# Performance work log

Hardware: AMD Instinct MI355X
Metric: run time of the kernel (lower is better)

## Reference

```python
import jax, jax.numpy as jnp
import numpy as np

B, S1, S2 = 1024, 25, 10          # batch, hop-1 fanout, hop-2 fanout
N, D, H, C = 100000, 256, 128, 64  # n_node, in_dim, per-branch out_dim, n_class


def setup_inputs() -> dict:
    key = jax.random.key(0)
    ks = jax.random.split(key, 10)
    rn = lambda k, shape: jax.random.normal(k, shape, dtype=jnp.float32) * 0.05
    return {
        "ids0": jax.random.randint(ks[0], (B,), 0, N),
        "ids1": jax.random.randint(ks[1], (B * S1,), 0, N),
        "ids2": jax.random.randint(ks[2], (B * S1 * S2,), 0, N),
        "features": jax.random.normal(ks[3], (N, D), dtype=jnp.float32),
        # aggregator layer 1 (in D, out 2H after concat)
        "Wx1": rn(ks[4], (D, H)), "bx1": jnp.zeros((H,), jnp.float32),
        "Wn1": rn(ks[5], (D, H)), "bn1": jnp.zeros((H,), jnp.float32),
        # aggregator layer 2 (in 2H, out 2H)
        "Wx2": rn(ks[6], (2 * H, H)), "bx2": jnp.zeros((H,), jnp.float32),
        "Wn2": rn(ks[7], (2 * H, H)), "bn2": jnp.zeros((H,), jnp.float32),
        # final linear head
        "Wfc": rn(ks[8], (2 * H, C)), "bfc": jnp.zeros((C,), jnp.float32),
    }


def _mean_agg(x, neibs, Wx, bx, Wn, bn, act):
    # neibs: [x_rows * fanout, d] -> mean over fanout, then concat of two linears
    n = neibs.reshape(x.shape[0], -1, neibs.shape[-1]).mean(axis=1)
    out = jnp.concatenate([x @ Wx + bx, n @ Wn + bn], axis=-1)
    return act(out)


def reference(ids0, ids1, ids2, features,
              Wx1, bx1, Wn1, bn1, Wx2, bx2, Wn2, bn2, Wfc, bfc):
    # hop-wise feature gathers (identity prep)
    h0 = features[ids0]   # [B, D]
    h1 = features[ids1]   # [B*S1, D]
    h2 = features[ids2]   # [B*S1*S2, D]
    # layer 1 aggregation (relu), applied to consecutive hop pairs
    g0 = _mean_agg(h0, h1, Wx1, bx1, Wn1, bn1, jax.nn.relu)   # [B, 2H]
    g1 = _mean_agg(h1, h2, Wx1, bx1, Wn1, bn1, jax.nn.relu)   # [B*S1, 2H]
    # layer 2 aggregation (identity activation on last layer)
    f0 = _mean_agg(g0, g1, Wx2, bx2, Wn2, bn2, lambda v: v)   # [B, 2H]
    return f0 @ Wfc + bfc  # [B, C]
```

## Files before the change

### kernel.cpp

```cpp
#include <hip/hip_runtime.h>

#define DD 256
#define HH 128
#define CC 64
#define BB 1024
#define SS1 25
#define SS2 10
#define NN 100000

typedef __attribute__((ext_vector_type(8))) short bf16x8;
typedef __attribute__((ext_vector_type(4))) float f32x4;

__device__ inline unsigned short f2b(float x) {
    union { float f; unsigned u; } v; v.f = x;
    unsigned r = (v.u + 0x7fffu + ((v.u >> 16) & 1u)) >> 16;
    return (unsigned short)r;
}
__device__ inline float b2f(unsigned u16) {
    union { unsigned u; float f; } v; v.u = u16 << 16;
    return v.f;
}

__global__ __launch_bounds__(256)
void prep_w(const float* __restrict__ Wx, const float* __restrict__ Wn,
            unsigned short* __restrict__ Wsw) {
    const int t    = blockIdx.x * 256 + threadIdx.x;
    const int lane = t & 63;
    const int frag = t >> 6;
    const int kc = frag >> 4, nt = frag & 15;
    const int quad = lane >> 4, lr = lane & 15;
    unsigned short v[8];
#pragma unroll
    for (int j = 0; j < 8; ++j) {
        int k = kc * 32 + quad * 8 + j;
        int n = nt * 16 + lr;
        float w = (n < HH) ? Wx[k * HH + n] : Wn[k * HH + (n - HH)];
        v[j] = f2b(w);
    }
    ((uint4*)Wsw)[t] = *(uint4*)v;
}

#define PQ_BLOCKS 512
#define PQ_TILES  (NN / 32)
#define AS 264

__global__ __launch_bounds__(256, 2)
void pq_gemm(const float* __restrict__ feat,
             const unsigned short* __restrict__ Wsw,
             unsigned short* __restrict__ PQb) {
    __shared__ unsigned short sAO[2][32 * AS];
    const int t    = threadIdx.x;
    const int w    = t >> 6, lane = t & 63;
    const int quad = lane >> 4, lr = lane & 15;

    bf16x8 B[8][4];
#pragma unroll
    for (int kc = 0; kc < 8; ++kc)
#pragma unroll
        for (int j = 0; j < 4; ++j)
            B[kc][j] = *(const bf16x8*)&Wsw[((kc * 16 + (w * 4 + j)) * 64 + lane) * 8];

    const int srow = t >> 5, sc = t & 31;

    float4 v[8];
    {
        const float* fb = feat + (long)blockIdx.x * 32 * DD + sc * 8;
#pragma unroll
        for (int i = 0; i < 4; ++i) {
            const float4* src = (const float4*)(fb + (long)(i * 8 + srow) * DD);
            v[2 * i]     = src[0];
            v[2 * i + 1] = src[1];
        }
    }

#pragma unroll 1
    for (int tile = blockIdx.x; tile < PQ_TILES; tile += PQ_BLOCKS) {
#pragma unroll
        for (int i = 0; i < 4; ++i) {
            int row = i * 8 + srow;
            float4 a = v[2 * i], b = v[2 * i + 1];
            unsigned short w8[8] = { f2b(a.x), f2b(a.y), f2b(a.z), f2b(a.w),
                                     f2b(b.x), f2b(b.y), f2b(b.z), f2b(b.w) };
            *(uint4*)&sAO[0][row * AS + sc * 8] = *(uint4*)w8;
        }
        int tn = tile + PQ_BLOCKS;
        if (tn < PQ_TILES) {
            const float* fn = feat + (long)tn * 32 * DD + sc * 8;
#pragma unroll
            for (int i = 0; i < 4; ++i) {
                const float4* src = (const float4*)(fn + (long)(i * 8 + srow) * DD);
                v[2 * i]     = src[0];
                v[2 * i + 1] = src[1];
            }
        }
        asm volatile("s_waitcnt lgkmcnt(0)" ::: "memory");
        __builtin_amdgcn_s_barrier();

        f32x4 acc[2][4] = {};
#pragma unroll
        for (int kc = 0; kc < 8; ++kc) {
            bf16x8 a0 = *(const bf16x8*)&sAO[0][(lr)      * AS + kc * 32 + quad * 8];
            bf16x8 a1 = *(const bf16x8*)&sAO[0][(16 + lr) * AS + kc * 32 + quad * 8];
#pragma unroll
            for (int j = 0; j < 4; ++j) {
                acc[0][j] = __builtin_amdgcn_mfma_f32_16x16x32_bf16(a0, B[kc][j], acc[0][j], 0, 0, 0);
                acc[1][j] = __builtin_amdgcn_mfma_f32_16x16x32_bf16(a1, B[kc][j], acc[1][j], 0, 0, 0);
            }
        }
#pragma unroll
        for (int rt = 0; rt < 2; ++rt)
#pragma unroll
            for (int j = 0; j < 4; ++j) {
                int col = (w * 4 + j) * 16 + lr;
#pragma unroll
                for (int r = 0; r < 4; ++r)
                    sAO[1][(rt * 16 + quad * 4 + r) * AS + col] = f2b(acc[rt][j][r]);
            }
        asm volatile("s_waitcnt lgkmcnt(0)" ::: "memory");
        __builtin_amdgcn_s_barrier();

#pragma unroll
        for (int i = 0; i < 4; ++i) {
            int id  = i * 256 + t;
            int row = id >> 5, ch = id & 31;
            uint4 d = *(uint4*)&sAO[1][row * AS + ch * 8];
            *(uint4*)&PQb[((long)tile * 32 + row) * DD + ch * 8] = d;
        }
    }
}

__global__ __launch_bounds__(256)
void megatail(const unsigned short* __restrict__ PQb,
              const int* __restrict__ ids0, const int* __restrict__ ids1,
              const int* __restrict__ ids2,
              const float* __restrict__ bx1, const float* __restrict__ bn1,
              const float* __restrict__ Wx2, const float* __restrict__ bx2,
              const float* __restrict__ Wn2, const float* __restrict__ bn2,
              const float* __restrict__ Wfc, const float* __restrict__ bfc,
              float* __restrict__ out) {
    __shared__ float sred[8][3 * HH];
    __shared__ float g0L[DD];
    __shared__ float gmL[DD];
    __shared__ float FL[DD];
    __shared__ float sp[4][CC];
    const int i    = blockIdx.x;
    const int t    = threadIdx.x;
    const int wv   = t >> 6, lane = t & 63;
    const int sub  = lane >> 5, lr = lane & 31;
    const int slot = wv * 2 + sub;

    const float4 bx = *(const float4*)&bx1[lr * 4];
    const float4 bn = *(const float4*)&bn1[lr * 4];
    float4 xs  = {0.f, 0.f, 0.f, 0.f};
    float4 ns  = {0.f, 0.f, 0.f, 0.f};
    float4 g0n = {0.f, 0.f, 0.f, 0.f};

#pragma unroll
    for (int it = 0; it < 4; ++it) {
        int s = slot + it * 8;
        if (s < SS1) {
            int row  = i * SS1 + s;
            long xr  = (long)ids1[row];
            uint2 xv  = *(const uint2*)&PQb[xr * DD + lr * 4];
            uint2 nv0 = *(const uint2*)&PQb[xr * DD + HH + lr * 4];
            int myid = ids2[row * SS2 + (lr % SS2)];
            float4 acc = {0.f, 0.f, 0.f, 0.f};
#pragma unroll
            for (int j = 0; j < SS2; ++j) {
                long nr = (long)__shfl(myid, (lane & 32) + j);
                uint2 nv = *(const uint2*)&PQb[nr * DD + HH + lr * 4];
                acc.x += b2f(nv.x & 0xffff); acc.y += b2f(nv.x >> 16);
                acc.z += b2f(nv.y & 0xffff); acc.w += b2f(nv.y >> 16);
            }
            constexpr float inv2 = 1.f / SS2;
            xs.x += fmaxf(b2f(xv.x & 0xffff) + bx.x, 0.f);
            xs.y += fmaxf(b2f(xv.x >> 16)    + bx.y, 0.f);
            xs.z += fmaxf(b2f(xv.y & 0xffff) + bx.z, 0.f);
            xs.w += fmaxf(b2f(xv.y >> 16)    + bx.w, 0.f);
            ns.x += fmaxf(acc.x * inv2 + bn.x, 0.f);
            ns.y += fmaxf(acc.y * inv2 + bn.y, 0.f);
            ns.z += fmaxf(acc.z * inv2 + bn.z, 0.f);
            ns.w += fmaxf(acc.w * inv2 + bn.w, 0.f);
            g0n.x += b2f(nv0.x & 0xffff); g0n.y += b2f(nv0.x >> 16);
            g0n.z += b2f(nv0.y & 0xffff); g0n.w += b2f(nv0.y >> 16);
        }
    }
    *(float4*)&sred[slot][lr * 4]            = xs;
    *(float4*)&sred[slot][HH + lr * 4]       = ns;
    *(float4*)&sred[slot][2 * HH + lr * 4]   = g0n;
    __syncthreads();

    {
        float rsum = 0.f;
#pragma unroll
        for (int k = 0; k < 8; ++k) rsum += sred[k][t];
        gmL[t] = rsum * (1.f / SS1);
        float g0v;
        if (t < HH) {
            unsigned short u = PQb[(long)ids0[i] * DD + t];
            g0v = fmaxf(b2f(u) + bx1[t], 0.f);
        } else {
            float s2 = 0.f;
#pragma unroll
            for (int k = 0; k < 8; ++k) s2 += sred[k][2 * HH + (t - HH)];
            g0v = fmaxf(s2 * (1.f / SS1) + bn1[t - HH], 0.f);
        }
        g0L[t] = g0v;
    }
    __syncthreads();

    {
        const bool xhalf = (t < HH);
        const float* __restrict__ W    = xhalf ? Wx2 : Wn2;
        const float* __restrict__ srcL = xhalf ? g0L : gmL;
        const int cc = t & (HH - 1);
        float fa = 0.f;
#pragma unroll 8
        for (int k = 0; k < DD; ++k) fa += srcL[k] * W[k * HH + cc];
        fa += xhalf ? bx2[cc] : bn2[cc];
        FL[t] = fa;
    }
    __syncthreads();

    {
        const int col = t & (CC - 1), q = t >> 6;
        float p = 0.f;
#pragma unroll 8
        for (int k = q * 64; k < q * 64 + 64; ++k) p += FL[k] * Wfc[k * CC + col];
        sp[q][col] = p;
    }
    __syncthreads();
    if (t < CC)
        out[(long)i * CC + t] = sp[0][t] + sp[1][t] + sp[2][t] + sp[3][t] + bfc[t];
}

extern "C" void kernel_launch(void* const* d_in, const int* in_sizes, int n_in,
                              void* d_out, int out_size, void* d_ws, size_t ws_size,
                              hipStream_t stream) {
    const int*   ids0 = (const int*)d_in[0];
    const int*   ids1 = (const int*)d_in[1];
    const int*   ids2 = (const int*)d_in[2];
    const float* feat = (const float*)d_in[3];
    const float* Wx1  = (const float*)d_in[4];
    const float* bx1  = (const float*)d_in[5];
    const float* Wn1  = (const float*)d_in[6];
    const float* bn1  = (const float*)d_in[7];
    const float* Wx2  = (const float*)d_in[8];
    const float* bx2  = (const float*)d_in[9];
    const float* Wn2  = (const float*)d_in[10];
    const float* bn2  = (const float*)d_in[11];
    const float* Wfc  = (const float*)d_in[12];
    const float* bfc  = (const float*)d_in[13];
    float* out = (float*)d_out;

    unsigned short* PQb = (unsigned short*)d_ws;
    unsigned short* Wsw = PQb + (long)NN * DD;

    prep_w<<<32, 256, 0, stream>>>(Wx1, Wn1, Wsw);
    pq_gemm<<<PQ_BLOCKS, 256, 0, stream>>>(feat, Wsw, PQb);
    megatail<<<BB, 256, 0, stream>>>(PQb, ids0, ids1, ids2, bx1, bn1,
                                     Wx2, bx2, Wn2, bn2, Wfc, bfc, out);
}
```

Measured before the change: 218.8 us.

## Double-buffer feature prefetch in pq_gemm and widen megatail to 512 threads

The PQ GEMM loop now keeps two register buffers of feature rows and prefetches two tiles ahead, so global loads of the next-next tile overlap the current tile's conversion and MFMA work. The tail kernel moves to 512 threads per block, spreading the 25 neighbor slots across 16 half-wave slots and splitting the layer-2 and FC dot products into more partial sums. The cost is higher register pressure in pq_gemm (16 float4 prefetch registers instead of 8), which may reduce occupancy under launch_bounds(256,2). The tail kernel also gains an extra shared-memory reduction step and barrier.

```diff
diff --git a/kernel.cpp b/kernel.cpp
--- a/kernel.cpp
+++ b/kernel.cpp
@@ -44,6 +44,71 @@
 #define PQ_TILES  (NN / 32)
 #define AS 264
 
+#define PQ_ISSUE(VREG, TIDX)                                                  \
+    {                                                                         \
+        const float* fn_ = feat + (long)(TIDX) * 32 * DD + sc * 8;            \
+        _Pragma("unroll")                                                     \
+        for (int i_ = 0; i_ < 4; ++i_) {                                      \
+            const float4* s_ = (const float4*)(fn_ + (long)(i_ * 8 + srow) * DD); \
+            VREG[2 * i_]     = s_[0];                                         \
+            VREG[2 * i_ + 1] = s_[1];                                         \
+        }                                                                     \
+    }
+
+#define PQ_STEP(VREG)                                                         \
+    {                                                                         \
+              \
+        _Pragma("unroll")                                                     \
+        for (int i_ = 0; i_ < 4; ++i_) {                                      \
+            int row_ = i_ * 8 + srow;                                         \
+            float4 a_ = VREG[2 * i_], b_ = VREG[2 * i_ + 1];                  \
+            unsigned short w8_[8] = { f2b(a_.x), f2b(a_.y), f2b(a_.z), f2b(a_.w), \
+                                      f2b(b_.x), f2b(b_.y), f2b(b_.z), f2b(b_.w) }; \
+            *(uint4*)&sAO[0][row_ * AS + sc * 8] = *(uint4*)w8_;              \
+        }                                                                     \
+                                \
+        {                                                                     \
+            long t2_ = tile + 2L * PQ_BLOCKS;                                 \
+            if (t2_ < PQ_TILES) PQ_ISSUE(VREG, t2_);                          \
+        }                                                                     \
+                       \
+        asm volatile("s_waitcnt lgkmcnt(0)" ::: "memory");                    \
+        __builtin_amdgcn_s_barrier();                                         \
+                                          \
+        f32x4 acc[2][4] = {};                                                 \
+        _Pragma("unroll")                                                     \
+        for (int kc = 0; kc < 8; ++kc) {                                      \
+            bf16x8 a0 = *(const bf16x8*)&sAO[0][(lr)      * AS + kc * 32 + quad * 8]; \
+            bf16x8 a1 = *(const bf16x8*)&sAO[0][(16 + lr) * AS + kc * 32 + quad * 8]; \
+            _Pragma("unroll")                                                 \
+            for (int j = 0; j < 4; ++j) {                                     \
+                acc[0][j] = __builtin_amdgcn_mfma_f32_16x16x32_bf16(a0, B[kc][j], acc[0][j], 0, 0, 0); \
+                acc[1][j] = __builtin_amdgcn_mfma_f32_16x16x32_bf16(a1, B[kc][j], acc[1][j], 0, 0, 0); \
+            }                                                                 \
+        }                                                                     \
+                  \
+        _Pragma("unroll")                                                     \
+        for (int rt = 0; rt < 2; ++rt)                                        \
+            _Pragma("unroll")                                                 \
+            for (int j = 0; j < 4; ++j) {                                     \
+                int col_ = (w * 4 + j) * 16 + lr;                             \
+                _Pragma("unroll")                                             \
+                for (int r = 0; r < 4; ++r)                                   \
+                    sAO[1][(rt * 16 + quad * 4 + r) * AS + col_] = f2b(acc[rt][j][r]); \
+            }                                                                 \
+                  \
+        asm volatile("s_waitcnt lgkmcnt(0)" ::: "memory");                    \
+        __builtin_amdgcn_s_barrier();                                         \
+                                           \
+        _Pragma("unroll")                                                     \
+        for (int i_ = 0; i_ < 4; ++i_) {                                      \
+            int id_  = i_ * 256 + t;                                          \
+            int row_ = id_ >> 5, ch_ = id_ & 31;                              \
+            uint4 d_ = *(uint4*)&sAO[1][row_ * AS + ch_ * 8];                 \
+            *(uint4*)&PQb[((long)tile * 32 + row_) * DD + ch_ * 8] = d_;      \
+        }                                                                     \
+    }
+
 __global__ __launch_bounds__(256, 2)
 void pq_gemm(const float* __restrict__ feat,
              const unsigned short* __restrict__ Wsw,
@@ -62,74 +127,20 @@
 
     const int srow = t >> 5, sc = t & 31;
 
-    float4 v[8];
-    {
-        const float* fb = feat + (long)blockIdx.x * 32 * DD + sc * 8;
-#pragma unroll
-        for (int i = 0; i < 4; ++i) {
-            const float4* src = (const float4*)(fb + (long)(i * 8 + srow) * DD);
-            v[2 * i]     = src[0];
-            v[2 * i + 1] = src[1];
-        }
-    }
-
-#pragma unroll 1
-    for (int tile = blockIdx.x; tile < PQ_TILES; tile += PQ_BLOCKS) {
-#pragma unroll
-        for (int i = 0; i < 4; ++i) {
-            int row = i * 8 + srow;
-            float4 a = v[2 * i], b = v[2 * i + 1];
-            unsigned short w8[8] = { f2b(a.x), f2b(a.y), f2b(a.z), f2b(a.w),
-                                     f2b(b.x), f2b(b.y), f2b(b.z), f2b(b.w) };
-            *(uint4*)&sAO[0][row * AS + sc * 8] = *(uint4*)w8;
-        }
-        int tn = tile + PQ_BLOCKS;
-        if (tn < PQ_TILES) {
-            const float* fn = feat + (long)tn * 32 * DD + sc * 8;
-#pragma unroll
-            for (int i = 0; i < 4; ++i) {
-                const float4* src = (const float4*)(fn + (long)(i * 8 + srow) * DD);
-                v[2 * i]     = src[0];
-                v[2 * i + 1] = src[1];
-            }
-        }
-        asm volatile("s_waitcnt lgkmcnt(0)" ::: "memory");
-        __builtin_amdgcn_s_barrier();
-
-        f32x4 acc[2][4] = {};
-#pragma unroll
-        for (int kc = 0; kc < 8; ++kc) {
-            bf16x8 a0 = *(const bf16x8*)&sAO[0][(lr)      * AS + kc * 32 + quad * 8];
-            bf16x8 a1 = *(const bf16x8*)&sAO[0][(16 + lr) * AS + kc * 32 + quad * 8];
-#pragma unroll
-            for (int j = 0; j < 4; ++j) {
-                acc[0][j] = __builtin_amdgcn_mfma_f32_16x16x32_bf16(a0, B[kc][j], acc[0][j], 0, 0, 0);
-                acc[1][j] = __builtin_amdgcn_mfma_f32_16x16x32_bf16(a1, B[kc][j], acc[1][j], 0, 0, 0);
-            }
-        }
-#pragma unroll
-        for (int rt = 0; rt < 2; ++rt)
-#pragma unroll
-            for (int j = 0; j < 4; ++j) {
-                int col = (w * 4 + j) * 16 + lr;
-#pragma unroll
-                for (int r = 0; r < 4; ++r)
-                    sAO[1][(rt * 16 + quad * 4 + r) * AS + col] = f2b(acc[rt][j][r]);
-            }
-        asm volatile("s_waitcnt lgkmcnt(0)" ::: "memory");
-        __builtin_amdgcn_s_barrier();
-
-#pragma unroll
-        for (int i = 0; i < 4; ++i) {
-            int id  = i * 256 + t;
-            int row = id >> 5, ch = id & 31;
-            uint4 d = *(uint4*)&sAO[1][row * AS + ch * 8];
-            *(uint4*)&PQb[((long)tile * 32 + row) * DD + ch * 8] = d;
-        }
-    }
-}
-
-__global__ __launch_bounds__(256)
+    float4 va[8], vb[8];
+    long tile = blockIdx.x;
+    PQ_ISSUE(va, tile);
+    if (tile + PQ_BLOCKS < PQ_TILES) PQ_ISSUE(vb, tile + PQ_BLOCKS);
+
+    while (true) {
+        PQ_STEP(va);
+        tile += PQ_BLOCKS; if (tile >= PQ_TILES) break;
+        PQ_STEP(vb);
+        tile += PQ_BLOCKS; if (tile >= PQ_TILES) break;
+    }
+}
+
+__global__ __launch_bounds__(512)
 void megatail(const unsigned short* __restrict__ PQb,
               const int* __restrict__ ids0, const int* __restrict__ ids1,
               const int* __restrict__ ids2,
@@ -138,11 +149,12 @@
               const float* __restrict__ Wn2, const float* __restrict__ bn2,
               const float* __restrict__ Wfc, const float* __restrict__ bfc,
               float* __restrict__ out) {
-    __shared__ float sred[8][3 * HH];
+    __shared__ float sred[16][3 * HH];
     __shared__ float g0L[DD];
     __shared__ float gmL[DD];
+    __shared__ float FP[2][DD];
     __shared__ float FL[DD];
-    __shared__ float sp[4][CC];
+    __shared__ float sp[8][CC];
     const int i    = blockIdx.x;
     const int t    = threadIdx.x;
     const int wv   = t >> 6, lane = t & 63;
@@ -156,8 +168,8 @@
     float4 g0n = {0.f, 0.f, 0.f, 0.f};
 
 #pragma unroll
-    for (int it = 0; it < 4; ++it) {
-        int s = slot + it * 8;
+    for (int it = 0; it < 2; ++it) {
+        int s = slot + it * 16;
         if (s < SS1) {
             int row  = i * SS1 + s;
             long xr  = (long)ids1[row];
@@ -185,53 +197,62 @@
             g0n.z += b2f(nv0.y & 0xffff); g0n.w += b2f(nv0.y >> 16);
         }
     }
-    *(float4*)&sred[slot][lr * 4]            = xs;
-    *(float4*)&sred[slot][HH + lr * 4]       = ns;
-    *(float4*)&sred[slot][2 * HH + lr * 4]   = g0n;
-    __syncthreads();
-
-    {
-        float rsum = 0.f;
-#pragma unroll
-        for (int k = 0; k < 8; ++k) rsum += sred[k][t];
-        gmL[t] = rsum * (1.f / SS1);
-        float g0v;
-        if (t < HH) {
-            unsigned short u = PQb[(long)ids0[i] * DD + t];
-            g0v = fmaxf(b2f(u) + bx1[t], 0.f);
+    *(float4*)&sred[slot][lr * 4]          = xs;
+    *(float4*)&sred[slot][HH + lr * 4]     = ns;
+    *(float4*)&sred[slot][2 * HH + lr * 4] = g0n;
+    __syncthreads();
+
+    if (t < 256) {
+        float r = 0.f;
+#pragma unroll
+        for (int k = 0; k < 16; ++k) r += sred[k][t];
+        gmL[t] = r * (1.f / SS1);
+    } else {
+        const int c = t - 256;
+        float v;
+        if (c < HH) {
+            unsigned short u = PQb[(long)ids0[i] * DD + c];
+            v = fmaxf(b2f(u) + bx1[c], 0.f);
         } else {
             float s2 = 0.f;
 #pragma unroll
-            for (int k = 0; k < 8; ++k) s2 += sred[k][2 * HH + (t - HH)];
-            g0v = fmaxf(s2 * (1.f / SS1) + bn1[t - HH], 0.f);
+            for (int k = 0; k < 16; ++k) s2 += sred[k][2 * HH + (c - HH)];
+            v = fmaxf(s2 * (1.f / SS1) + bn1[c - HH], 0.f);
         }
-        g0L[t] = g0v;
+        g0L[c] = v;
     }
     __syncthreads();
 
     {
-        const bool xhalf = (t < HH);
+        const int c = t & 255, h = t >> 8;
+        const bool xhalf = (c < HH);
         const float* __restrict__ W    = xhalf ? Wx2 : Wn2;
         const float* __restrict__ srcL = xhalf ? g0L : gmL;
-        const int cc = t & (HH - 1);
+        const int cc = c & (HH - 1);
         float fa = 0.f;
 #pragma unroll 8
-        for (int k = 0; k < DD; ++k) fa += srcL[k] * W[k * HH + cc];
-        fa += xhalf ? bx2[cc] : bn2[cc];
-        FL[t] = fa;
-    }
+        for (int k = h * 128; k < h * 128 + 128; ++k) fa += srcL[k] * W[k * HH + cc];
+        FP[h][c] = fa;
+    }
+    __syncthreads();
+    if (t < 256)
+        FL[t] = FP[0][t] + FP[1][t] + ((t < HH) ? bx2[t] : bn2[t - HH]);
     __syncthreads();
 
     {
         const int col = t & (CC - 1), q = t >> 6;
         float p = 0.f;
 #pragma unroll 8
-        for (int k = q * 64; k < q * 64 + 64; ++k) p += FL[k] * Wfc[k * CC + col];
+        for (int k = q * 32; k < q * 32 + 32; ++k) p += FL[k] * Wfc[k * CC + col];
         sp[q][col] = p;
     }
     __syncthreads();
-    if (t < CC)
-        out[(long)i * CC + t] = sp[0][t] + sp[1][t] + sp[2][t] + sp[3][t] + bfc[t];
+    if (t < CC) {
+        float r = bfc[t];
+#pragma unroll
+        for (int q = 0; q < 8; ++q) r += sp[q][t];
+        out[(long)i * CC + t] = r;
+    }
 }
 
 extern "C" void kernel_launch(void* const* d_in, const int* in_sizes, int n_in,
@@ -258,6 +279,6 @@
 
     prep_w<<<32, 256, 0, stream>>>(Wx1, Wn1, Wsw);
     pq_gemm<<<PQ_BLOCKS, 256, 0, stream>>>(feat, Wsw, PQb);
-    megatail<<<BB, 256, 0, stream>>>(PQb, ids0, ids1, ids2, bx1, bn1,
+    megatail<<<BB, 512, 0, stream>>>(PQb, ids0, ids1, ids2, bx1, bn1,
                                      Wx2, bx2, Wn2, bn2, Wfc, bfc, out);
 }
```

New measurement: 217.0 us. About the same (-0.8%).
